# Optimization experiments

Measured on AMD Instinct MI355X. Metric: run time of the kernel, lower is better.

## Reference

```python
import jax, jax.numpy as jnp
import numpy as np

B, S, D, H = 2, 2048, 2048, 16
HD = D // H  # 128
L = 10  # adapter_len


def setup_inputs() -> dict:
    key = jax.random.key(0)
    ks = jax.random.split(key, 8)
    x = jax.random.normal(ks[0], (B, S, D), dtype=jnp.float32)
    wq = jax.random.normal(ks[1], (D, D), dtype=jnp.float32) * 0.02
    wk = jax.random.normal(ks[2], (D, D), dtype=jnp.float32) * 0.02
    wv = jax.random.normal(ks[3], (D, D), dtype=jnp.float32) * 0.02
    wo = jax.random.normal(ks[4], (D, D), dtype=jnp.float32) * 0.02
    adapter = jax.random.normal(ks[5], (1, L, D), dtype=jnp.float32)
    gate = jax.random.normal(ks[6], (1, H, 1, 1), dtype=jnp.float32) * 0.1
    # rotary frequencies (LLaMA style, theta=10000)
    inv_freq = 1.0 / (10000.0 ** (jnp.arange(0, HD, 2, dtype=jnp.float32) / HD))
    t = jnp.arange(S, dtype=jnp.float32)
    ang = jnp.outer(t, inv_freq)  # [S, HD//2]
    freqs_cos = jnp.cos(ang)
    freqs_sin = jnp.sin(ang)
    # additive causal mask [1,1,S,S]
    mask = jnp.triu(jnp.full((S, S), -1e9, dtype=jnp.float32), k=1)[None, None]
    return {"x": x, "wq": wq, "wk": wk, "wv": wv, "wo": wo,
            "adapter": adapter, "gate": gate,
            "freqs_cos": freqs_cos, "freqs_sin": freqs_sin, "mask": mask}


def _rope(v, cos, sin):
    # v: [B,S,H,HD]; cos/sin: [S, HD//2]; complex multiply on (even, odd) pairs
    v = v.reshape(*v.shape[:-1], HD // 2, 2)
    v0, v1 = v[..., 0], v[..., 1]
    c = cos[None, :, None, :]
    s = sin[None, :, None, :]
    out = jnp.stack([v0 * c - v1 * s, v0 * s + v1 * c], axis=-1)
    return out.reshape(*out.shape[:-2], HD)


def reference(x, wq, wk, wv, wo, adapter, gate, freqs_cos, freqs_sin, mask):
    scale = 1.0 / np.sqrt(HD)
    xq = (x @ wq).reshape(B, S, H, HD)
    xk = (x @ wk).reshape(B, S, H, HD)
    xv = (x @ wv).reshape(B, S, H, HD)
    xq = _rope(xq, freqs_cos, freqs_sin)
    xk = _rope(xk, freqs_cos, freqs_sin)
    # self-attention with additive causal mask
    scores = jnp.einsum('bqhd,bkhd->bhqk', xq, xk) * scale + mask
    probs = jax.nn.softmax(scores.astype(jnp.float32), axis=-1).astype(xq.dtype)
    out = jnp.einsum('bhqk,bkhd->bqhd', probs, xv)  # [B,S,H,HD]
    # gated adapter cross-attention (no rotary on adapter K/V)
    ak = (adapter[0] @ wk).reshape(L, H, HD)
    av = (adapter[0] @ wv).reshape(L, H, HD)
    a_scores = jnp.einsum('bqhd,khd->bhqk', xq, ak) * scale
    a_probs = gate * jax.nn.softmax(a_scores.astype(jnp.float32), axis=-1).astype(xq.dtype)
    out = out + jnp.einsum('bhqk,khd->bqhd', a_probs, av)
    return out.reshape(B, S, D) @ wo
```

## Files before the change

### kernel.cpp

```cpp
#include <hip/hip_runtime.h>


typedef unsigned short ushort_t;
typedef unsigned int uint32;
typedef __attribute__((ext_vector_type(8))) short bf16x8;
typedef __attribute__((ext_vector_type(4))) float f32x4;

__device__ __forceinline__ void async16(void* lds, const void* g) {
  __builtin_amdgcn_global_load_lds((const __attribute__((address_space(1))) void*)g,
                                   (__attribute__((address_space(3))) void*)lds,
                                   16, 0, 0);
}
__device__ __forceinline__ ushort_t f2bf(float f) {
  uint32 u = __float_as_uint(f);
  u += 0x7FFFu + ((u >> 16) & 1u);
  return (ushort_t)(u >> 16);
}
__device__ __forceinline__ float bf2f(ushort_t b) {
  return __uint_as_float(((uint32)b) << 16);
}
__device__ __forceinline__ float dpp_xor1(float v) {
  return __int_as_float(__builtin_amdgcn_update_dpp(
      0, __float_as_int(v), 0xB1, 0xf, 0xf, true));
}
#define DPP_MAX(t, ctrl) \
  t = fmaxf(t, __int_as_float(__builtin_amdgcn_update_dpp( \
      0, __float_as_int(t), (ctrl), 0xf, 0xf, true)))
#define DPP_ADD(t, ctrl) \
  t += __int_as_float(__builtin_amdgcn_update_dpp( \
      0, __float_as_int(t), (ctrl), 0xf, 0xf, true))
__device__ __forceinline__ float rowmax16(float t) {
  DPP_MAX(t, 0xB1);
  DPP_MAX(t, 0x4E);
  t = fmaxf(t, __int_as_float(__builtin_amdgcn_ds_swizzle(
      __float_as_int(t), 0x101F)));
  DPP_MAX(t, 0x128);
  return t;
}
__device__ __forceinline__ float rowsum16(float t) {
  DPP_ADD(t, 0xB1);
  DPP_ADD(t, 0x4E);
  t += __int_as_float(__builtin_amdgcn_ds_swizzle(__float_as_int(t), 0x101F));
  DPP_ADD(t, 0x128);
  return t;
}

__global__ __launch_bounds__(256) void cast_x_kernel(const float* __restrict__ x,
                                                     ushort_t* __restrict__ Xb) {
  size_t i = ((size_t)blockIdx.x * 256 + threadIdx.x) * 8;
  float4 a = *(const float4*)(x + i);
  float4 b = *(const float4*)(x + i + 4);
  uint4 o;
  o.x = (uint32)f2bf(a.x) | ((uint32)f2bf(a.y) << 16);
  o.y = (uint32)f2bf(a.z) | ((uint32)f2bf(a.w) << 16);
  o.z = (uint32)f2bf(b.x) | ((uint32)f2bf(b.y) << 16);
  o.w = (uint32)f2bf(b.z) | ((uint32)f2bf(b.w) << 16);
  *(uint4*)(Xb + i) = o;
}

__global__ __launch_bounds__(256) void rope_pack_kernel(
    const float* __restrict__ fc, const float* __restrict__ fs,
    float2* __restrict__ fcs) {
  int i = blockIdx.x * 256 + threadIdx.x;
  fcs[i] = make_float2(fc[i], fs[i]);
}

__global__ __launch_bounds__(256) void transpose_w_kernel(
    const float* __restrict__ w0, const float* __restrict__ w1,
    const float* __restrict__ w2, const float* __restrict__ w3,
    ushort_t* __restrict__ outBase) {
  const float* W = (blockIdx.z == 0) ? w0 : (blockIdx.z == 1) ? w1
                 : (blockIdx.z == 2) ? w2 : w3;
  ushort_t* Wt = outBase + (size_t)blockIdx.z * 4194304;
  __shared__ float L[64][65];
  int t = threadIdx.x, tc = t & 63, tr = t >> 6;
  int k0 = blockIdx.x * 64, n0 = blockIdx.y * 64;
  for (int i = 0; i < 16; ++i) {
    int r = i * 4 + tr;
    L[r][tc] = W[(size_t)(k0 + r) * 2048 + n0 + tc];
  }
  __syncthreads();
  int tr8 = t >> 5, tc2 = t & 31;
  for (int i = 0; i < 8; ++i) {
    int r = i * 8 + tr8;
    uint32 pk = (uint32)f2bf(L[2 * tc2][r]) | ((uint32)f2bf(L[2 * tc2 + 1][r]) << 16);
    *(uint32*)(Wt + (size_t)(n0 + r) * 2048 + k0 + 2 * tc2) = pk;
  }
}

__global__ __launch_bounds__(256) void adapter_kv_kernel(
    const float* __restrict__ adapter, const float* __restrict__ wk,
    const float* __restrict__ wv, float* __restrict__ ak, float* __restrict__ av) {
  const float* W = blockIdx.z ? wv : wk;
  float* out = blockIdx.z ? av : ak;
  __shared__ float As[10][128];
  int t = threadIdx.x;
  int k0 = blockIdx.y * 128;
  for (int i = t; i < 1280; i += 256)
    As[i >> 7][i & 127] = adapter[(size_t)(i >> 7) * 2048 + k0 + (i & 127)];
  __syncthreads();
  int n = blockIdx.x * 256 + t;
  float acc[10];
#pragma unroll
  for (int l = 0; l < 10; ++l) acc[l] = 0.f;
  for (int kk = 0; kk < 128; ++kk) {
    float wv_ = W[(size_t)(k0 + kk) * 2048 + n];
#pragma unroll
    for (int l = 0; l < 10; ++l) acc[l] += As[l][kk] * wv_;
  }
#pragma unroll
  for (int l = 0; l < 10; ++l) atomicAdd(&out[l * 2048 + n], acc[l]);
}

__global__ __launch_bounds__(256) void adapter_pack_kernel(
    const float* __restrict__ ak, const float* __restrict__ av,
    ushort_t* __restrict__ akb, ushort_t* __restrict__ avb) {
  int t = blockIdx.x * 256 + threadIdx.x;
  if (t < 32768) {
    int h = t >> 11, l = (t >> 7) & 15, d = t & 127;
    akb[t] = (l < 10) ? f2bf(ak[l * 2048 + h * 128 + d]) : (ushort_t)0;
  }
  int h = t >> 12, d = (t >> 5) & 127, l = t & 31;
  avb[t] = (l < 10) ? f2bf(av[l * 2048 + h * 128 + d]) : (ushort_t)0;
}

#define QK_BARX() asm volatile("s_barrier" ::: "memory")
#define QK_LGKM0() asm volatile("s_waitcnt lgkmcnt(0)" ::: "memory")

__device__ __forceinline__ void kloop_128x256(
    char* lds, const ushort_t* __restrict__ A, const ushort_t* __restrict__ Bt,
    size_t bm0, size_t bn0, f32x4 (&acc)[4][4]) {
  const int tid = (int)threadIdx.x;
  const int w = tid >> 6, lane = tid & 63, quad = lane >> 4, l15 = lane & 15;
  const int wr = (w >> 2) * 64, wc = (w & 3) * 64;
  const int nt = 32;
  char* const pA0 = lds;
  char* const pA1 = lds + 16384;
  char* const pB0 = lds + 32768;
  char* const pB1 = lds + 65536;

#define PAT(T) (((T) & 1) ? pA1 : pA0)
#define PBT(T) (((T) & 1) ? pB1 : pB0)
#define SEGL(OP, LDSB, GROW, T)                                                \
  do {                                                                         \
    int rr_ = w * 8 + (lane >> 3);                                             \
    int cl_ = (lane & 7) ^ (rr_ & 7);                                          \
    async16((LDSB) + w * 1024,                                                 \
            (OP) + ((GROW) + (size_t)rr_) * 2048 + (size_t)((T) * 64 + cl_ * 8)); \
  } while (0)
#define ST_A(T)                                                                \
  do { if ((T) < nt) { SEGL(A, PAT(T), bm0, (T));                              \
                       SEGL(A, PAT(T) + 8192, bm0 + 64, (T)); } } while (0)
#define ST_B0(T)                                                               \
  do { if ((T) < nt) SEGL(Bt, PBT(T), bn0, (T)); } while (0)
#define ST_B123(T)                                                             \
  do { if ((T) < nt) { SEGL(Bt, PBT(T) + 8192,  bn0 + 64,  (T));               \
                       SEGL(Bt, PBT(T) + 16384, bn0 + 128, (T));               \
                       SEGL(Bt, PBT(T) + 24576, bn0 + 192, (T)); } } while (0)

  ST_A(0); ST_B0(0); ST_B123(0); ST_B123(1);
  asm volatile("s_waitcnt vmcnt(3)" ::: "memory");
  QK_BARX();

#pragma unroll 2
  for (int t = 0; t < nt; ++t) {
    const char* pA = PAT(t);
    const char* pB = PBT(t);
    bf16x8 bfv[4][2];
#pragma unroll
    for (int j = 0; j < 4; ++j) {
      int brow = wc + j * 16 + l15;
#pragma unroll
      for (int ks = 0; ks < 2; ++ks)
        bfv[j][ks] = *(const bf16x8*)(pB + brow * 128 +
                                      (((ks * 4 + quad) ^ (brow & 7)) * 16));
    }
#pragma unroll
    for (int ph = 0; ph < 2; ++ph) {
      bf16x8 af[2][2];
#pragma unroll
      for (int ii = 0; ii < 2; ++ii) {
        int arow = wr + (ph * 2 + ii) * 16 + l15;
#pragma unroll
        for (int ks = 0; ks < 2; ++ks)
          af[ii][ks] = *(const bf16x8*)(pA + arow * 128 +
                                        (((ks * 4 + quad) ^ (arow & 7)) * 16));
      }
      if (ph == 0) { ST_A(t + 1); ST_B0(t + 1); }
      else         { ST_B123(t + 2); }
      QK_BARX();
      QK_LGKM0();
      __builtin_amdgcn_s_setprio(1);
#pragma unroll
      for (int ks = 0; ks < 2; ++ks)
#pragma unroll
        for (int ii = 0; ii < 2; ++ii)
#pragma unroll
          for (int j = 0; j < 4; ++j)
            acc[ph * 2 + ii][j] = __builtin_amdgcn_mfma_f32_16x16x32_bf16(
                af[ii][ks], bfv[j][ks], acc[ph * 2 + ii][j], 0, 0, 0);
      __builtin_amdgcn_s_setprio(0);
      if (ph == 1) {
        if (t == nt - 2) asm volatile("s_waitcnt vmcnt(0)" ::: "memory");
        else             asm volatile("s_waitcnt vmcnt(3)" ::: "memory");
      }
      QK_BARX();
    }
  }
#undef PAT
#undef PBT
#undef SEGL
#undef ST_A
#undef ST_B0
#undef ST_B123
}

__global__ __launch_bounds__(512, 2) void gemm_qkv128_kernel(
    const ushort_t* __restrict__ A, const ushort_t* __restrict__ Bt,
    ushort_t* __restrict__ outQ, ushort_t* __restrict__ outK,
    ushort_t* __restrict__ Vt, const float2* __restrict__ fcs) {
  __shared__ char lds[98304];
  const int tid = (int)threadIdx.x;
  const int w = tid >> 6, lane = tid & 63, quad = lane >> 4, l15 = lane & 15;
  const int wr = (w >> 2) * 64, wc = (w & 3) * 64;

  const int wg = ((int)blockIdx.x & 7) * 96 + ((int)blockIdx.x >> 3);
  const size_t bm0 = (size_t)(wg & 31) * 128;
  const size_t bn0 = (size_t)(wg >> 5) * 256;

  f32x4 acc[4][4];
  f32x4 z4 = {0.f, 0.f, 0.f, 0.f};
#pragma unroll
  for (int i = 0; i < 4; ++i)
#pragma unroll
    for (int j = 0; j < 4; ++j) acc[i][j] = z4;

  kloop_128x256(lds, A, Bt, bm0, bn0, acc);

  const int seg = (int)(bn0 >> 11);
  if (seg < 2) {
    ushort_t* ob = seg ? outK : outQ;
#pragma unroll
    for (int i = 0; i < 4; ++i)
#pragma unroll
      for (int r = 0; r < 4; ++r) {
        size_t m = bm0 + wr + i * 16 + quad * 4 + r;
        int s = (int)(m & 2047);
#pragma unroll
        for (int j = 0; j < 4; ++j) {
          size_t n = (bn0 + wc + j * 16 + l15) & 2047;
          float v = acc[i][j][r];
          float v2 = dpp_xor1(v);
          int fi = ((int)n & 127) >> 1;
          float2 cs = fcs[s * 64 + fi];
          v = (lane & 1) ? (v2 * cs.y + v * cs.x) : (v * cs.x - v2 * cs.y);
          ob[m * 2048 + n] = f2bf(v);
        }
      }
  } else {
    char* T = lds + w * 8192;
#pragma unroll
    for (int i = 0; i < 4; ++i)
#pragma unroll
      for (int j = 0; j < 4; ++j) {
        int nn = j * 16 + l15;
        int md0 = i * 8 + quad * 2;
        uint32 p01 = (uint32)f2bf(acc[i][j][0]) | ((uint32)f2bf(acc[i][j][1]) << 16);
        uint32 p23 = (uint32)f2bf(acc[i][j][2]) | ((uint32)f2bf(acc[i][j][3]) << 16);
        *(uint32*)(T + nn * 128 + ((md0 ^ (nn & 31)) * 4)) = p01;
        *(uint32*)(T + nn * 128 + (((md0 + 1) ^ (nn & 31)) * 4)) = p23;
      }
    const int b = (int)(bm0 >> 11);
    const int s0 = (int)(bm0 & 2047) + wr;
    const int n2 = (int)(bn0 & 2047) + wc;
#pragma unroll
    for (int it = 0; it < 32; ++it) {
      int row = it * 2 + (lane >> 5);
      int pp = lane & 31;
      uint32 dv = *(const uint32*)(T + row * 128 + pp * 4);
      int md = pp ^ (row & 31);
      int nloc = n2 + row;
      size_t bh = (size_t)b * 16 + (nloc >> 7);
      *(uint32*)(Vt + (bh * 128 + (size_t)(nloc & 127)) * 2048 + s0 + 2 * md) = dv;
    }
  }
}

__global__ __launch_bounds__(512, 2) void gemm_wo_kernel(
    const ushort_t* __restrict__ A, const ushort_t* __restrict__ Bt,
    float* __restrict__ out) {
  __shared__ char lds[98304];
  const int tid = (int)threadIdx.x;
  const int w = tid >> 6, lane = tid & 63, quad = lane >> 4, l15 = lane & 15;
  const int wr = (w >> 2) * 64, wc = (w & 3) * 64;

  const int wg = ((int)blockIdx.x & 7) * 32 + ((int)blockIdx.x >> 3);
  const size_t bm0 = (size_t)(wg & 31) * 128;
  const size_t bn0 = (size_t)(wg >> 5) * 256;

  f32x4 acc[4][4];
  f32x4 z4 = {0.f, 0.f, 0.f, 0.f};
#pragma unroll
  for (int i = 0; i < 4; ++i)
#pragma unroll
    for (int j = 0; j < 4; ++j) acc[i][j] = z4;

  kloop_128x256(lds, A, Bt, bm0, bn0, acc);

#pragma unroll
  for (int i = 0; i < 4; ++i)
#pragma unroll
    for (int r = 0; r < 4; ++r) {
      size_t m = bm0 + wr + i * 16 + quad * 4 + r;
#pragma unroll
      for (int j = 0; j < 4; ++j) {
        size_t n = bn0 + wc + j * 16 + l15;
        out[m * 2048 + n] = acc[i][j][r];
      }
    }
}

__global__ __launch_bounds__(256, 4) void flash_kernel(
    const ushort_t* __restrict__ Qb, const ushort_t* __restrict__ Kb,
    const ushort_t* __restrict__ Vt, const ushort_t* __restrict__ akb,
    const ushort_t* __restrict__ avb, const float* __restrict__ gate,
    ushort_t* __restrict__ Ob) {
  __shared__ char ldsK[16384];
  __shared__ char ldsV[16384];
  __shared__ char ldsP[8192];
  const int tid = threadIdx.x;
  const int w = tid >> 6, lane = tid & 63, quad = lane >> 4, l15 = lane & 15;
  const int idx = blockIdx.x;
  const int pg = idx >> 8, c = idx & 255;
  const int u = c >> 3, vv = c & 7;
  const int uu = (pg & 2) ? ((u + 16) & 31) : u;
  const int qt2 = (pg & 1) ? (31 - uu) : uu;
  const int hb = (pg << 3) | vv;
  const int h = hb >> 1, b = hb & 1;
  const float scale = 0.08838834764831845f;

  bf16x8 ones;
#pragma unroll
  for (int j = 0; j < 8; ++j) ones[j] = (short)0x3F80;

  bf16x8 qf[4];
  {
    size_t qrow = (size_t)qt2 * 64 + w * 16 + l15;
    const ushort_t* base = Qb + ((size_t)b * 2048 + qrow) * 2048 + h * 128 + quad * 8;
#pragma unroll
    for (int ds = 0; ds < 4; ++ds) qf[ds] = *(const bf16x8*)(base + ds * 32);
  }

  f32x4 zero4 = {0.f, 0.f, 0.f, 0.f};
  f32x4 oacc[8];
  f32x4 osum = zero4;
  float mrow[4];
#pragma unroll
  for (int n8 = 0; n8 < 8; ++n8) oacc[n8] = zero4;
#pragma unroll
  for (int r = 0; r < 4; ++r) mrow[r] = -1e30f;

  for (int kt = 0; kt <= qt2; ++kt) {
#pragma unroll
    for (int ii = 0; ii < 4; ++ii) {
      int r0 = w * 16 + ii * 4;
      int row = r0 + (lane >> 4);
      int cl = (lane & 15) ^ (row & 15);
      async16(ldsK + r0 * 256,
              Kb + ((size_t)b * 2048 + kt * 64 + row) * 2048 + h * 128 + cl * 8);
    }
#pragma unroll
    for (int ii = 0; ii < 4; ++ii) {
      int d0 = w * 32 + ii * 8;
      int dr = d0 + (lane >> 3);
      int cl = (lane & 7) ^ (dr & 7);
      async16(ldsV + d0 * 128,
              Vt + ((size_t)(b * 16 + h) * 128 + dr) * 2048 + kt * 64 + cl * 8);
    }
    __syncthreads();

    f32x4 sacc[4];
#pragma unroll
    for (int nt = 0; nt < 4; ++nt) sacc[nt] = zero4;
#pragma unroll
    for (int ds = 0; ds < 4; ++ds) {
      bf16x8 kf[4];
      int ch = ds * 4 + quad;
#pragma unroll
      for (int nt = 0; nt < 4; ++nt) {
        int row = nt * 16 + l15;
        kf[nt] = *(const bf16x8*)(ldsK + row * 256 + ((ch ^ (row & 15)) * 16));
      }
#pragma unroll
      for (int nt = 0; nt < 4; ++nt)
        sacc[nt] = __builtin_amdgcn_mfma_f32_16x16x32_bf16(qf[ds], kf[nt], sacc[nt], 0, 0, 0);
    }

    const bool domask = (kt == qt2);
    float tmax[4] = {-1e30f, -1e30f, -1e30f, -1e30f};
    const int qbr = qt2 * 64 + w * 16 + quad * 4;
#pragma unroll
    for (int nt = 0; nt < 4; ++nt) {
      int kg = kt * 64 + nt * 16 + l15;
#pragma unroll
      for (int r = 0; r < 4; ++r) {
        float s = sacc[nt][r] * scale;
        if (domask && kg > qbr + r) s = -1e30f;
        sacc[nt][r] = s;
        tmax[r] = fmaxf(tmax[r], s);
      }
    }
    float need = 0.f;
#pragma unroll
    for (int r = 0; r < 4; ++r) {
      tmax[r] = rowmax16(tmax[r]);
      need = fmaxf(need, tmax[r] - mrow[r]);
    }
    if (__any(need > 8.0f)) {
      float alpha[4];
#pragma unroll
      for (int r = 0; r < 4; ++r) {
        float mnew = fmaxf(mrow[r], tmax[r]);
        alpha[r] = __expf(mrow[r] - mnew);
        osum[r] *= alpha[r];
        mrow[r] = mnew;
      }
#pragma unroll
      for (int n8 = 0; n8 < 8; ++n8)
#pragma unroll
        for (int r = 0; r < 4; ++r) oacc[n8][r] *= alpha[r];
    }
    uint32 pk[4][4];
#pragma unroll
    for (int nt = 0; nt < 4; ++nt)
#pragma unroll
      for (int r = 0; r < 4; ++r) {
        float pv = __expf(sacc[nt][r] - mrow[r]);
        float pn = dpp_xor1(pv);
        uint32 d_;
        asm volatile("v_cvt_pk_bf16_f32 %0, %1, %2" : "=v"(d_) : "v"(pv), "v"(pn));
        pk[nt][r] = d_;
      }
    if (!(lane & 1)) {
#pragma unroll
      for (int nt = 0; nt < 4; ++nt)
#pragma unroll
        for (int r = 0; r < 4; ++r) {
          int col = nt * 16 + l15;
          int prow = w * 16 + quad * 4 + r;
          *(uint32*)(ldsP + prow * 128 + (((col >> 3) ^ (prow & 7)) * 16) + (col & 7) * 2) = pk[nt][r];
        }
    }

#pragma unroll
    for (int ks = 0; ks < 2; ++ks) {
      int ch = ks * 4 + quad;
      int prow = w * 16 + l15;
      bf16x8 pf = *(const bf16x8*)(ldsP + prow * 128 + ((ch ^ (prow & 7)) * 16));
      osum = __builtin_amdgcn_mfma_f32_16x16x32_bf16(pf, ones, osum, 0, 0, 0);
#pragma unroll
      for (int n8 = 0; n8 < 8; ++n8) {
        int dr = n8 * 16 + l15;
        bf16x8 vf = *(const bf16x8*)(ldsV + dr * 128 + ((ch ^ (dr & 7)) * 16));
        oacc[n8] = __builtin_amdgcn_mfma_f32_16x16x32_bf16(pf, vf, oacc[n8], 0, 0, 0);
      }
    }
    __syncthreads();
  }

  const float g = gate[h];
  {
    int row = w * 16 + (lane >> 2);
    *(uint2*)(ldsP + row * 80 + 32 + (lane & 3) * 8) = make_uint2(0, 0);
  }
  f32x4 sa = zero4;
#pragma unroll
  for (int ds = 0; ds < 4; ++ds) {
    bf16x8 kfa = *(const bf16x8*)(akb + ((size_t)h * 16 + l15) * 128 + ds * 32 + quad * 8);
    sa = __builtin_amdgcn_mfma_f32_16x16x32_bf16(qf[ds], kfa, sa, 0, 0, 0);
  }
#pragma unroll
  for (int r = 0; r < 4; ++r) {
    float s = sa[r] * scale;
    if (l15 >= 10) s = -1e30f;
    float mx = rowmax16(s);
    float e = __expf(s - mx);
    float sum = rowsum16(e);
    float pv = g * e / sum;
    int row = w * 16 + quad * 4 + r;
    *(ushort_t*)(ldsP + row * 80 + l15 * 2) = f2bf(pv);
  }
  bf16x8 paf = *(const bf16x8*)(ldsP + (w * 16 + l15) * 80 + quad * 16);

  float rl[4];
#pragma unroll
  for (int r = 0; r < 4; ++r) rl[r] = 1.f / osum[r];
#pragma unroll
  for (int n8 = 0; n8 < 8; ++n8)
#pragma unroll
    for (int r = 0; r < 4; ++r) oacc[n8][r] *= rl[r];
#pragma unroll
  for (int n8 = 0; n8 < 8; ++n8) {
    bf16x8 avf = *(const bf16x8*)(avb + ((size_t)h * 128 + n8 * 16 + l15) * 32 + quad * 8);
    oacc[n8] = __builtin_amdgcn_mfma_f32_16x16x32_bf16(paf, avf, oacc[n8], 0, 0, 0);
  }
  size_t qb0 = (size_t)qt2 * 64 + w * 16 + quad * 4;
#pragma unroll
  for (int n8 = 0; n8 < 8; ++n8) {
    size_t col = (size_t)h * 128 + n8 * 16 + l15;
#pragma unroll
    for (int r = 0; r < 4; ++r)
      Ob[((size_t)b * 2048 + qb0 + r) * 2048 + col] = f2bf(oacc[n8][r]);
  }
}

extern "C" void kernel_launch(void* const* d_in, const int* in_sizes, int n_in,
                              void* d_out, int out_size, void* d_ws, size_t ws_size,
                              hipStream_t stream) {
  (void)in_sizes; (void)n_in; (void)out_size; (void)ws_size;
  const float* x       = (const float*)d_in[0];
  const float* wq      = (const float*)d_in[1];
  const float* wk      = (const float*)d_in[2];
  const float* wv      = (const float*)d_in[3];
  const float* wo      = (const float*)d_in[4];
  const float* adapter = (const float*)d_in[5];
  const float* gate    = (const float*)d_in[6];
  const float* fc      = (const float*)d_in[7];
  const float* fs      = (const float*)d_in[8];

  char* ws = (char*)d_ws;
  ushort_t* Xb   = (ushort_t*)(ws + 0);
  ushort_t* WtQ  = (ushort_t*)(ws + 16777216);
  ushort_t* WtO  = (ushort_t*)(ws + 41943040);
  ushort_t* Qb   = (ushort_t*)(ws + 50331648);
  ushort_t* Kb   = (ushort_t*)(ws + 67108864);
  ushort_t* Vt   = (ushort_t*)(ws + 83886080);
  float*    ak   = (float*)   (ws + 100663296);
  float*    av   = (float*)   (ws + 100745216);
  ushort_t* akb  = (ushort_t*)(ws + 100827136);
  ushort_t* avb  = (ushort_t*)(ws + 100892672);
  float2*   fcs  = (float2*)  (ws + 101023744);
  ushort_t* Ob   = Xb;

  cast_x_kernel<<<4096, 256, 0, stream>>>(x, Xb);
  rope_pack_kernel<<<512, 256, 0, stream>>>(fc, fs, fcs);
  transpose_w_kernel<<<dim3(32, 32, 4), 256, 0, stream>>>(wq, wk, wv, wo, WtQ);
  hipMemsetAsync(ak, 0, 163840, stream);
  adapter_kv_kernel<<<dim3(8, 16, 2), 256, 0, stream>>>(adapter, wk, wv, ak, av);
  adapter_pack_kernel<<<256, 256, 0, stream>>>(ak, av, akb, avb);
  gemm_qkv128_kernel<<<dim3(768), 512, 0, stream>>>(Xb, WtQ, Qb, Kb, Vt, fcs);
  flash_kernel<<<dim3(1024), 256, 0, stream>>>(Qb, Kb, Vt, akb, avb, gate, Ob);
  gemm_wo_kernel<<<dim3(256), 512, 0, stream>>>(Ob, WtO, (float*)d_out);
}
```

Measured before the change: 432.6 us.

## Use 256x256 tiles for QKV GEMM and drop rope packing kernel

Replaces the 128x256-tile QKV projection GEMM with a 256x256-tile kernel. It uses a new double-buffered, split-K-half LDS pipeline that interleaves async global-to-LDS loads with four MFMA phases per K step, so each loaded tile is reused more. The separate rope cos/sin packing kernel is removed and the epilogue reads fc/fs directly, saving one launch. The cost is 128KB of LDS per block and twice the accumulators per thread, which may reduce occupancy. Only 384 workgroups are launched, which may leave the MI355X's 256 CUs unevenly loaded.

```diff
diff --git a/kernel.cpp b/kernel.cpp
--- a/kernel.cpp
+++ b/kernel.cpp
@@ -58,13 +58,6 @@
   *(uint4*)(Xb + i) = o;
 }
 
-__global__ __launch_bounds__(256) void rope_pack_kernel(
-    const float* __restrict__ fc, const float* __restrict__ fs,
-    float2* __restrict__ fcs) {
-  int i = blockIdx.x * 256 + threadIdx.x;
-  fcs[i] = make_float2(fc[i], fs[i]);
-}
-
 __global__ __launch_bounds__(256) void transpose_w_kernel(
     const float* __restrict__ w0, const float* __restrict__ w1,
     const float* __restrict__ w2, const float* __restrict__ w3,
@@ -126,6 +119,170 @@
 
 #define QK_BARX() asm volatile("s_barrier" ::: "memory")
 #define QK_LGKM0() asm volatile("s_waitcnt lgkmcnt(0)" ::: "memory")
+
+__global__ __launch_bounds__(512, 2) void gemm_qkv256_kernel(
+    const ushort_t* __restrict__ A, const ushort_t* __restrict__ Bt,
+    ushort_t* __restrict__ outQ, ushort_t* __restrict__ outK,
+    ushort_t* __restrict__ Vt,
+    const float* __restrict__ fc, const float* __restrict__ fs) {
+  __shared__ char lds[131072];
+  const int tid = (int)threadIdx.x;
+  const int w = tid >> 6, lane = tid & 63, quad = lane >> 4, l15 = lane & 15;
+  const int wr = w >> 2, wc = w & 3;
+  const int nt = 32;
+
+  const int wg = ((int)blockIdx.x & 7) * 48 + ((int)blockIdx.x >> 3);
+  const size_t bm0 = (size_t)(wg & 15) * 256;
+  const size_t bn0 = (size_t)(wg >> 4) * 256;
+
+#define SEGH(OB, G, GROW, T, KH)                                               \
+  do { if ((T) < nt) {                                                         \
+    int c_ = lane & 3;                                                         \
+    _Pragma("unroll") for (int L_ = 0; L_ < 2; ++L_) {                         \
+      int r_ = L_ * 128 + w * 16 + (lane >> 2);                                \
+      async16(lds + (OB) + (((T) & 1) * 32768) + (KH) * 16384 + L_ * 8192 + w * 1024, \
+              (G) + ((GROW) + (size_t)r_) * 2048 +                             \
+                  (size_t)((T) * 64 + (KH) * 32 + ((c_ ^ (r_ & 3)) * 8)));     \
+    } } } while (0)
+#define FRAG(OB, BUF, KS, RA) \
+  (*(const bf16x8*)(lds + (OB) + (BUF) + (KS) * 16384 + (RA) * 64 + \
+                    ((quad ^ ((RA) & 3)) * 16)))
+
+  f32x4 acc[8][4];
+  f32x4 z4 = {0.f, 0.f, 0.f, 0.f};
+#pragma unroll
+  for (int i = 0; i < 8; ++i)
+#pragma unroll
+    for (int j = 0; j < 4; ++j) acc[i][j] = z4;
+
+  SEGH(0, A, bm0, 0, 0); SEGH(65536, Bt, bn0, 0, 0);
+  SEGH(0, A, bm0, 0, 1); SEGH(65536, Bt, bn0, 0, 1);
+  SEGH(0, A, bm0, 1, 0); SEGH(65536, Bt, bn0, 1, 0);
+  asm volatile("s_waitcnt vmcnt(4)" ::: "memory");
+  QK_BARX();
+
+  for (int t = 0; t < nt; ++t) {
+    const int buf = (t & 1) * 32768;
+    bf16x8 af[4], bfv[4];
+
+#pragma unroll
+    for (int j = 0; j < 4; ++j) bfv[j] = FRAG(65536, buf, 0, wc * 64 + j * 16 + l15);
+#pragma unroll
+    for (int i = 0; i < 4; ++i) af[i] = FRAG(0, buf, 0, wr * 128 + i * 16 + l15);
+    SEGH(0, A, bm0, t + 1, 1);
+    QK_BARX();
+    QK_LGKM0();
+    __builtin_amdgcn_s_setprio(1);
+#pragma unroll
+    for (int i = 0; i < 4; ++i)
+#pragma unroll
+      for (int j = 0; j < 4; ++j)
+        acc[i][j] = __builtin_amdgcn_mfma_f32_16x16x32_bf16(af[i], bfv[j], acc[i][j], 0, 0, 0);
+    __builtin_amdgcn_s_setprio(0);
+    QK_BARX();
+
+#pragma unroll
+    for (int i = 0; i < 4; ++i) af[i] = FRAG(0, buf, 0, wr * 128 + (4 + i) * 16 + l15);
+    SEGH(65536, Bt, bn0, t + 1, 1);
+    QK_BARX();
+    QK_LGKM0();
+    __builtin_amdgcn_s_setprio(1);
+#pragma unroll
+    for (int i = 0; i < 4; ++i)
+#pragma unroll
+      for (int j = 0; j < 4; ++j)
+        acc[4 + i][j] = __builtin_amdgcn_mfma_f32_16x16x32_bf16(af[i], bfv[j], acc[4 + i][j], 0, 0, 0);
+    __builtin_amdgcn_s_setprio(0);
+    QK_BARX();
+
+#pragma unroll
+    for (int j = 0; j < 4; ++j) bfv[j] = FRAG(65536, buf, 1, wc * 64 + j * 16 + l15);
+#pragma unroll
+    for (int i = 0; i < 4; ++i) af[i] = FRAG(0, buf, 1, wr * 128 + (4 + i) * 16 + l15);
+    SEGH(0, A, bm0, t + 2, 0);
+    QK_BARX();
+    QK_LGKM0();
+    __builtin_amdgcn_s_setprio(1);
+#pragma unroll
+    for (int i = 0; i < 4; ++i)
+#pragma unroll
+      for (int j = 0; j < 4; ++j)
+        acc[4 + i][j] = __builtin_amdgcn_mfma_f32_16x16x32_bf16(af[i], bfv[j], acc[4 + i][j], 0, 0, 0);
+    __builtin_amdgcn_s_setprio(0);
+    QK_BARX();
+
+#pragma unroll
+    for (int i = 0; i < 4; ++i) af[i] = FRAG(0, buf, 1, wr * 128 + i * 16 + l15);
+    SEGH(65536, Bt, bn0, t + 2, 0);
+    QK_BARX();
+    QK_LGKM0();
+    __builtin_amdgcn_s_setprio(1);
+#pragma unroll
+    for (int i = 0; i < 4; ++i)
+#pragma unroll
+      for (int j = 0; j < 4; ++j)
+        acc[i][j] = __builtin_amdgcn_mfma_f32_16x16x32_bf16(af[i], bfv[j], acc[i][j], 0, 0, 0);
+    __builtin_amdgcn_s_setprio(0);
+    if (t == nt - 2) asm volatile("s_waitcnt vmcnt(0)" ::: "memory");
+    else             asm volatile("s_waitcnt vmcnt(4)" ::: "memory");
+    QK_BARX();
+  }
+#undef SEGH
+#undef FRAG
+
+  const int seg = (int)(bn0 >> 11);
+  if (seg < 2) {
+    ushort_t* ob = seg ? outK : outQ;
+#pragma unroll
+    for (int i = 0; i < 8; ++i)
+#pragma unroll
+      for (int r = 0; r < 4; ++r) {
+        size_t m = bm0 + wr * 128 + i * 16 + quad * 4 + r;
+        int s = (int)(m & 2047);
+#pragma unroll
+        for (int j = 0; j < 4; ++j) {
+          size_t n = (bn0 + wc * 64 + j * 16 + l15) & 2047;
+          float v = acc[i][j][r];
+          float v2 = dpp_xor1(v);
+          int fi = ((int)n & 127) >> 1;
+          float cosv = fc[s * 64 + fi];
+          float sinv = fs[s * 64 + fi];
+          v = (lane & 1) ? (v2 * sinv + v * cosv) : (v * cosv - v2 * sinv);
+          ob[m * 2048 + n] = f2bf(v);
+        }
+      }
+  } else {
+    char* T = lds + w * 16384;
+    const int b = (int)(bm0 >> 11);
+    const int n2 = (int)(bn0 & 2047) + wc * 64;
+#pragma unroll
+    for (int mh = 0; mh < 2; ++mh) {
+#pragma unroll
+      for (int i = 0; i < 4; ++i)
+#pragma unroll
+        for (int j = 0; j < 4; ++j) {
+          int nn = j * 16 + l15;
+          int md0 = i * 8 + quad * 2;
+          const f32x4 av4 = acc[mh * 4 + i][j];
+          uint32 p01 = (uint32)f2bf(av4[0]) | ((uint32)f2bf(av4[1]) << 16);
+          uint32 p23 = (uint32)f2bf(av4[2]) | ((uint32)f2bf(av4[3]) << 16);
+          *(uint32*)(T + nn * 128 + ((md0 ^ (nn & 31)) * 4)) = p01;
+          *(uint32*)(T + nn * 128 + (((md0 + 1) ^ (nn & 31)) * 4)) = p23;
+        }
+      const int s0 = (int)(bm0 & 2047) + wr * 128 + mh * 64;
+#pragma unroll
+      for (int it = 0; it < 32; ++it) {
+        int row = it * 2 + (lane >> 5);
+        int pp = lane & 31;
+        uint32 dv = *(const uint32*)(T + row * 128 + pp * 4);
+        int md = pp ^ (row & 31);
+        int nloc = n2 + row;
+        size_t bh = (size_t)b * 16 + (nloc >> 7);
+        *(uint32*)(Vt + (bh * 128 + (size_t)(nloc & 127)) * 2048 + s0 + 2 * md) = dv;
+      }
+    }
+  }
+}
 
 __device__ __forceinline__ void kloop_128x256(
     char* lds, const ushort_t* __restrict__ A, const ushort_t* __restrict__ Bt,
@@ -215,77 +372,6 @@
 #undef ST_B123
 }
 
-__global__ __launch_bounds__(512, 2) void gemm_qkv128_kernel(
-    const ushort_t* __restrict__ A, const ushort_t* __restrict__ Bt,
-    ushort_t* __restrict__ outQ, ushort_t* __restrict__ outK,
-    ushort_t* __restrict__ Vt, const float2* __restrict__ fcs) {
-  __shared__ char lds[98304];
-  const int tid = (int)threadIdx.x;
-  const int w = tid >> 6, lane = tid & 63, quad = lane >> 4, l15 = lane & 15;
-  const int wr = (w >> 2) * 64, wc = (w & 3) * 64;
-
-  const int wg = ((int)blockIdx.x & 7) * 96 + ((int)blockIdx.x >> 3);
-  const size_t bm0 = (size_t)(wg & 31) * 128;
-  const size_t bn0 = (size_t)(wg >> 5) * 256;
-
-  f32x4 acc[4][4];
-  f32x4 z4 = {0.f, 0.f, 0.f, 0.f};
-#pragma unroll
-  for (int i = 0; i < 4; ++i)
-#pragma unroll
-    for (int j = 0; j < 4; ++j) acc[i][j] = z4;
-
-  kloop_128x256(lds, A, Bt, bm0, bn0, acc);
-
-  const int seg = (int)(bn0 >> 11);
-  if (seg < 2) {
-    ushort_t* ob = seg ? outK : outQ;
-#pragma unroll
-    for (int i = 0; i < 4; ++i)
-#pragma unroll
-      for (int r = 0; r < 4; ++r) {
-        size_t m = bm0 + wr + i * 16 + quad * 4 + r;
-        int s = (int)(m & 2047);
-#pragma unroll
-        for (int j = 0; j < 4; ++j) {
-          size_t n = (bn0 + wc + j * 16 + l15) & 2047;
-          float v = acc[i][j][r];
-          float v2 = dpp_xor1(v);
-          int fi = ((int)n & 127) >> 1;
-          float2 cs = fcs[s * 64 + fi];
-          v = (lane & 1) ? (v2 * cs.y + v * cs.x) : (v * cs.x - v2 * cs.y);
-          ob[m * 2048 + n] = f2bf(v);
-        }
-      }
-  } else {
-    char* T = lds + w * 8192;
-#pragma unroll
-    for (int i = 0; i < 4; ++i)
-#pragma unroll
-      for (int j = 0; j < 4; ++j) {
-        int nn = j * 16 + l15;
-        int md0 = i * 8 + quad * 2;
-        uint32 p01 = (uint32)f2bf(acc[i][j][0]) | ((uint32)f2bf(acc[i][j][1]) << 16);
-        uint32 p23 = (uint32)f2bf(acc[i][j][2]) | ((uint32)f2bf(acc[i][j][3]) << 16);
-        *(uint32*)(T + nn * 128 + ((md0 ^ (nn & 31)) * 4)) = p01;
-        *(uint32*)(T + nn * 128 + (((md0 + 1) ^ (nn & 31)) * 4)) = p23;
-      }
-    const int b = (int)(bm0 >> 11);
-    const int s0 = (int)(bm0 & 2047) + wr;
-    const int n2 = (int)(bn0 & 2047) + wc;
-#pragma unroll
-    for (int it = 0; it < 32; ++it) {
-      int row = it * 2 + (lane >> 5);
-      int pp = lane & 31;
-      uint32 dv = *(const uint32*)(T + row * 128 + pp * 4);
-      int md = pp ^ (row & 31);
-      int nloc = n2 + row;
-      size_t bh = (size_t)b * 16 + (nloc >> 7);
-      *(uint32*)(Vt + (bh * 128 + (size_t)(nloc & 127)) * 2048 + s0 + 2 * md) = dv;
-    }
-  }
-}
-
 __global__ __launch_bounds__(512, 2) void gemm_wo_kernel(
     const ushort_t* __restrict__ A, const ushort_t* __restrict__ Bt,
     float* __restrict__ out) {
@@ -539,16 +625,14 @@
   float*    av   = (float*)   (ws + 100745216);
   ushort_t* akb  = (ushort_t*)(ws + 100827136);
   ushort_t* avb  = (ushort_t*)(ws + 100892672);
-  float2*   fcs  = (float2*)  (ws + 101023744);
   ushort_t* Ob   = Xb;
 
   cast_x_kernel<<<4096, 256, 0, stream>>>(x, Xb);
-  rope_pack_kernel<<<512, 256, 0, stream>>>(fc, fs, fcs);
   transpose_w_kernel<<<dim3(32, 32, 4), 256, 0, stream>>>(wq, wk, wv, wo, WtQ);
   hipMemsetAsync(ak, 0, 163840, stream);
   adapter_kv_kernel<<<dim3(8, 16, 2), 256, 0, stream>>>(adapter, wk, wv, ak, av);
   adapter_pack_kernel<<<256, 256, 0, stream>>>(ak, av, akb, avb);
-  gemm_qkv128_kernel<<<dim3(768), 512, 0, stream>>>(Xb, WtQ, Qb, Kb, Vt, fcs);
+  gemm_qkv256_kernel<<<dim3(384), 512, 0, stream>>>(Xb, WtQ, Qb, Kb, Vt, fc, fs);
   flash_kernel<<<dim3(1024), 256, 0, stream>>>(Qb, Kb, Vt, akb, avb, gate, Ob);
   gemm_wo_kernel<<<dim3(256), 512, 0, stream>>>(Ob, WtO, (float*)d_out);
 }
```

Measured after the change: 454.8 us. 5.1% more time.
